# Optimization experiments

Hardware: AMD Instinct MI355X
Metric: run time of the kernel (lower is better)

Reference implementation:

```python
import jax, jax.numpy as jnp
import numpy as np

SIZE = 128
BATCH = 64
STEEPNESS = 10.0


def _odd_even_indices(n):
    """Odd-even transposition sorting network: n layers of disjoint adjacent pairs.
    All layers are padded to k = n//2 pairs with self-pairs (i,i)=(0,0), which are
    exact no-ops under the soft compare-exchange (matches pass-through wires of the
    original network)."""
    k = n // 2
    ia, ib = [], []
    for layer in range(n):
        start = layer % 2
        pa = list(range(start, n - 1, 2))
        pb = [i + 1 for i in pa]
        while len(pa) < k:  # pad with no-op self-pairs
            pa.append(0)
            pb.append(0)
        ia.append(pa)
        ib.append(pb)
    return jnp.asarray(np.array(ia, np.int32)), jnp.asarray(np.array(ib, np.int32))


def setup_inputs() -> dict:
    key = jax.random.key(0)
    return {"vectors": jax.random.normal(key, (BATCH, SIZE), dtype=jnp.float32)}


def _soft_sort(vectors):
    Bsz, n = vectors.shape
    ia, ib = _odd_even_indices(n)  # [n_layers, k] each
    x0 = vectors
    # X[b, i, j] = soft probability mass of input element i at output slot j,
    # i.e. the invariant  x[b] == vectors[b] @ X[b]  holds after every layer.
    X0 = jnp.tile(jnp.eye(n, dtype=vectors.dtype)[None], (Bsz, 1, 1))
    inv_pi = jnp.float32(1.0 / np.pi)

    def step(carry, idx):
        x, X = carry
        a_idx, b_idx = idx
        a = x[:, a_idx]  # [B, k]
        b = x[:, b_idx]  # [B, k]
        # Cauchy CDF relaxation of the comparison (module default distribution)
        alpha = jnp.arctan(STEEPNESS * (b - a)) * inv_pi + 0.5
        x = x.at[:, a_idx].set(alpha * a + (1.0 - alpha) * b)        # soft min
        x = x.at[:, b_idx].set((1.0 - alpha) * a + alpha * b)        # soft max
        A = X[:, :, a_idx]   # [B, n, k] columns feeding the 'a' wires
        Bc = X[:, :, b_idx]  # [B, n, k] columns feeding the 'b' wires
        w = alpha[:, None, :]
        X = X.at[:, :, a_idx].set(w * A + (1.0 - w) * Bc)
        X = X.at[:, :, b_idx].set((1.0 - w) * A + w * Bc)
        return (x, X), None

    (x, X), _ = jax.lax.scan(step, (x0, X0), (ia, ib))
    return x, X


def reference(vectors):
    # Returns (softly sorted values [B, n], relaxed permutation matrix [B, n, n])
    return _soft_sort(vectors)
```

## Files before the change

### kernel.cpp

```cpp
#include <hip/hip_runtime.h>
#include <math.h>

#define SIZE 128
#define BATCH 64
#define STEEP 10.0f
#define INV_PI 0.3183098861837907f

__global__ __launch_bounds__(256) void soft_sort_kernel(
    const float* __restrict__ vec, float* __restrict__ out)
{
    const int tid      = threadIdx.x;
    const int lane     = tid & 63;
    const int wave     = tid >> 6;
    const int batch    = blockIdx.x >> 2;
    const int rowchunk = blockIdx.x & 3;
    const int r_base   = rowchunk * 32 + wave * 8;

    const int c0 = 2 * lane;
    const int c1 = c0 + 1;

    const float2 xv = *reinterpret_cast<const float2*>(vec + batch * SIZE + c0);
    float xa = xv.x, xb = xv.y;

    float XA[8], XB[8];
#pragma unroll
    for (int i = 0; i < 8; ++i) {
        const int row = r_base + i;
        XA[i] = (row == c0) ? 1.0f : 0.0f;
        XB[i] = (row == c1) ? 1.0f : 0.0f;
    }

    const int laneR = (lane < 63) ? lane + 1 : 63;
    const int laneL = (lane > 0)  ? lane - 1 : 0;
    const bool hasR = (lane < 63);
    const bool hasL = (lane > 0);

    for (int layer = 0; layer < SIZE; layer += 2) {
        {
            const float alpha = atanf(STEEP * (xb - xa)) * INV_PI + 0.5f;
            const float t  = alpha * (xa - xb);
            const float na = xb + t;
            xb = xa - t;
            xa = na;
#pragma unroll
            for (int i = 0; i < 8; ++i) {
                const float tr = alpha * (XA[i] - XB[i]);
                const float nA = XB[i] + tr;
                XB[i] = XA[i] - tr;
                XA[i] = nA;
            }
        }
        {
            const float xnext  = __shfl(xa, laneR);
            const float alphaR = atanf(STEEP * (xnext - xb)) * INV_PI + 0.5f;
            const float alphaL = __shfl(alphaR, laneL);
            const float xprev  = __shfl(xb, laneL);

            const float nxb = xnext + alphaR * (xb - xnext);
            const float nxa = xprev + alphaL * (xa - xprev);
            xb = hasR ? nxb : xb;
            xa = hasL ? nxa : xa;
#pragma unroll
            for (int i = 0; i < 8; ++i) {
                const float nA = __shfl(XA[i], laneR);
                const float pB = __shfl(XB[i], laneL);
                const float nXB = nA + alphaR * (XB[i] - nA);
                const float nXA = pB + alphaL * (XA[i] - pB);
                XB[i] = hasR ? nXB : XB[i];
                XA[i] = hasL ? nXA : XA[i];
            }
        }
    }

    float* __restrict__ Xout = out + BATCH * SIZE + batch * SIZE * SIZE;
#pragma unroll
    for (int i = 0; i < 8; ++i) {
        const int row = r_base + i;
        *reinterpret_cast<float2*>(Xout + row * SIZE + c0) = make_float2(XA[i], XB[i]);
    }
    if (rowchunk == 0 && wave == 0) {
        *reinterpret_cast<float2*>(out + batch * SIZE + c0) = make_float2(xa, xb);
    }
}

extern "C" void kernel_launch(void* const* d_in, const int* in_sizes, int n_in,
                              void* d_out, int out_size, void* d_ws, size_t ws_size,
                              hipStream_t stream) {
    const float* vec = (const float*)d_in[0];
    float* out = (float*)d_out;
    (void)in_sizes; (void)n_in; (void)d_ws; (void)ws_size; (void)out_size;

    dim3 grid(BATCH * 4);
    dim3 block(256);
    hipLaunchKernelGGL(soft_sort_kernel, grid, block, 0, stream, vec, out);
}
```

Measured before the change: 79.46 us.

## Split soft sort into alpha precompute and permutation-evolution kernels with polynomial atan

A first kernel runs the value recurrence once per batch and stores all per-layer alphas in workspace, using a minimax polynomial atan approximation instead of atanf. A second kernel evolves the permutation rows with a new layout: each thread holds 8 contiguous columns, so most compare-exchanges happen in registers and only two shuffles are needed per odd layer. This removes the redundant alpha recomputation done by every row-chunk block and most of the cross-lane shuffles. The cost is an extra kernel launch, a global round-trip through the alpha buffer, and approximation error in alpha.

```diff
diff --git a/kernel.cpp b/kernel.cpp
--- a/kernel.cpp
+++ b/kernel.cpp
@@ -4,83 +4,129 @@
 #define SIZE 128
 #define BATCH 64
 #define STEEP 10.0f
-#define INV_PI 0.3183098861837907f
 
-__global__ __launch_bounds__(256) void soft_sort_kernel(
-    const float* __restrict__ vec, float* __restrict__ out)
+__device__ __forceinline__ float alpha_from_delta(float delta) {
+    const float C0 =  0.31830265f;
+    const float C1 = -0.10587730f;
+    const float C2 =  0.06160680f;
+    const float C3 = -0.03706173f;
+    const float C4 =  0.01676007f;
+    const float C5 = -0.00373098f;
+    float t   = STEEP * delta;
+    float at  = fabsf(t);
+    bool  inv = at > 1.0f;
+    float z   = inv ? __builtin_amdgcn_rcpf(at) : at;
+    float z2  = z * z;
+    float q   = C5;
+    q = fmaf(q, z2, C4);
+    q = fmaf(q, z2, C3);
+    q = fmaf(q, z2, C2);
+    q = fmaf(q, z2, C1);
+    q = fmaf(q, z2, C0);
+    q = q * z;
+    float r = inv ? 0.5f - q : q;
+    return (t >= 0.0f) ? (0.5f + r) : (0.5f - r);
+}
+
+__global__ __launch_bounds__(64) void alpha_kernel(
+    const float* __restrict__ vec, float* __restrict__ alpha_buf,
+    float* __restrict__ out)
 {
-    const int tid      = threadIdx.x;
-    const int lane     = tid & 63;
-    const int wave     = tid >> 6;
-    const int batch    = blockIdx.x >> 2;
-    const int rowchunk = blockIdx.x & 3;
-    const int r_base   = rowchunk * 32 + wave * 8;
-
-    const int c0 = 2 * lane;
-    const int c1 = c0 + 1;
+    const int lane  = threadIdx.x;
+    const int batch = blockIdx.x;
+    const int c0    = 2 * lane;
 
     const float2 xv = *reinterpret_cast<const float2*>(vec + batch * SIZE + c0);
     float xa = xv.x, xb = xv.y;
 
-    float XA[8], XB[8];
+    float* __restrict__ ab = alpha_buf + batch * (SIZE * 64);
+    const int  laneR = (lane < 63) ? lane + 1 : 63;
+    const int  laneL = (lane > 0)  ? lane - 1 : 0;
+    const bool hasR  = (lane < 63);
+    const bool hasL  = (lane > 0);
+
+    for (int layer = 0; layer < SIZE; layer += 2) {
+        const float ae = alpha_from_delta(xb - xa);
+        ab[layer * 64 + lane] = ae;
+        const float t  = ae * (xa - xb);
+        const float na = xb + t;
+        xb = xa - t;
+        xa = na;
+        const float xnext = __shfl(xa, laneR);
+        const float ao    = alpha_from_delta(xnext - xb);
+        ab[(layer + 1) * 64 + lane] = ao;
+        const float aoL   = __shfl(ao, laneL);
+        const float xprev = __shfl(xb, laneL);
+        const float nxb = xnext + ao  * (xb - xnext);
+        const float nxa = xprev + aoL * (xa - xprev);
+        xb = hasR ? nxb : xb;
+        xa = hasL ? nxa : xa;
+    }
+    *reinterpret_cast<float2*>(out + batch * SIZE + c0) = make_float2(xa, xb);
+}
+
+__global__ __launch_bounds__(256) void evolve_kernel(
+    const float* __restrict__ alpha_buf, float* __restrict__ out)
+{
+    const int tid     = threadIdx.x;
+    const int lane    = tid & 63;
+    const int wave    = tid >> 6;
+    const int chunk   = lane & 15;
+    const int row_sub = lane >> 4;
+    const int batch   = blockIdx.x >> 3;
+    const int rowgrp  = blockIdx.x & 7;
+    const int row     = rowgrp * 16 + wave * 4 + row_sub;
+    const int c8      = chunk * 8;
+
+    float v[8];
 #pragma unroll
-    for (int i = 0; i < 8; ++i) {
-        const int row = r_base + i;
-        XA[i] = (row == c0) ? 1.0f : 0.0f;
-        XB[i] = (row == c1) ? 1.0f : 0.0f;
+    for (int j = 0; j < 8; ++j) v[j] = (row == c8 + j) ? 1.0f : 0.0f;
+
+    const float* __restrict__ ab = alpha_buf + batch * (SIZE * 64);
+    const int q4 = chunk * 4;
+    const int qm = (q4 > 0) ? q4 - 1 : 0;
+
+    const bool hasR  = (chunk < 15);
+    const bool hasL  = (chunk > 0);
+    const int  laneR = hasR ? lane + 1 : lane;
+    const int  laneL = hasL ? lane - 1 : lane;
+
+    float4 ae = *reinterpret_cast<const float4*>(ab + 0 * 64 + q4);
+    float4 ao = *reinterpret_cast<const float4*>(ab + 1 * 64 + q4);
+    float  aL = ab[1 * 64 + qm];
+
+    for (int L = 0; L < 64; ++L) {
+        const int nxt = (L < 63) ? (2 * L + 2) : (2 * L);
+        const float4 ae_n = *reinterpret_cast<const float4*>(ab + nxt * 64 + q4);
+        const float4 ao_n = *reinterpret_cast<const float4*>(ab + (nxt + 1) * 64 + q4);
+        const float  aL_n = ab[(nxt + 1) * 64 + qm];
+
+        {
+            float A, B, d;
+            A = v[0]; B = v[1]; d = A - B; v[0] = fmaf(ae.x, d, B); v[1] = fmaf(-ae.x, d, A);
+            A = v[2]; B = v[3]; d = A - B; v[2] = fmaf(ae.y, d, B); v[3] = fmaf(-ae.y, d, A);
+            A = v[4]; B = v[5]; d = A - B; v[4] = fmaf(ae.z, d, B); v[5] = fmaf(-ae.z, d, A);
+            A = v[6]; B = v[7]; d = A - B; v[6] = fmaf(ae.w, d, B); v[7] = fmaf(-ae.w, d, A);
+        }
+        const float nb0 = __shfl(v[0], laneR);
+        const float pb7 = __shfl(v[7], laneL);
+        {
+            float A, B, d;
+            A = v[1]; B = v[2]; d = A - B; v[1] = fmaf(ao.x, d, B); v[2] = fmaf(-ao.x, d, A);
+            A = v[3]; B = v[4]; d = A - B; v[3] = fmaf(ao.y, d, B); v[4] = fmaf(-ao.y, d, A);
+            A = v[5]; B = v[6]; d = A - B; v[5] = fmaf(ao.z, d, B); v[6] = fmaf(-ao.z, d, A);
+        }
+        const float r = fmaf(ao.w, v[7] - nb0, nb0);
+        const float l = fmaf(aL, v[0] - pb7, pb7);
+        v[7] = hasR ? r : v[7];
+        v[0] = hasL ? l : v[0];
+
+        ae = ae_n; ao = ao_n; aL = aL_n;
     }
 
-    const int laneR = (lane < 63) ? lane + 1 : 63;
-    const int laneL = (lane > 0)  ? lane - 1 : 0;
-    const bool hasR = (lane < 63);
-    const bool hasL = (lane > 0);
-
-    for (int layer = 0; layer < SIZE; layer += 2) {
-        {
-            const float alpha = atanf(STEEP * (xb - xa)) * INV_PI + 0.5f;
-            const float t  = alpha * (xa - xb);
-            const float na = xb + t;
-            xb = xa - t;
-            xa = na;
-#pragma unroll
-            for (int i = 0; i < 8; ++i) {
-                const float tr = alpha * (XA[i] - XB[i]);
-                const float nA = XB[i] + tr;
-                XB[i] = XA[i] - tr;
-                XA[i] = nA;
-            }
-        }
-        {
-            const float xnext  = __shfl(xa, laneR);
-            const float alphaR = atanf(STEEP * (xnext - xb)) * INV_PI + 0.5f;
-            const float alphaL = __shfl(alphaR, laneL);
-            const float xprev  = __shfl(xb, laneL);
-
-            const float nxb = xnext + alphaR * (xb - xnext);
-            const float nxa = xprev + alphaL * (xa - xprev);
-            xb = hasR ? nxb : xb;
-            xa = hasL ? nxa : xa;
-#pragma unroll
-            for (int i = 0; i < 8; ++i) {
-                const float nA = __shfl(XA[i], laneR);
-                const float pB = __shfl(XB[i], laneL);
-                const float nXB = nA + alphaR * (XB[i] - nA);
-                const float nXA = pB + alphaL * (XA[i] - pB);
-                XB[i] = hasR ? nXB : XB[i];
-                XA[i] = hasL ? nXA : XA[i];
-            }
-        }
-    }
-
-    float* __restrict__ Xout = out + BATCH * SIZE + batch * SIZE * SIZE;
-#pragma unroll
-    for (int i = 0; i < 8; ++i) {
-        const int row = r_base + i;
-        *reinterpret_cast<float2*>(Xout + row * SIZE + c0) = make_float2(XA[i], XB[i]);
-    }
-    if (rowchunk == 0 && wave == 0) {
-        *reinterpret_cast<float2*>(out + batch * SIZE + c0) = make_float2(xa, xb);
-    }
+    float* __restrict__ X = out + BATCH * SIZE + (batch * SIZE + row) * SIZE + c8;
+    *reinterpret_cast<float4*>(X)     = make_float4(v[0], v[1], v[2], v[3]);
+    *reinterpret_cast<float4*>(X + 4) = make_float4(v[4], v[5], v[6], v[7]);
 }
 
 extern "C" void kernel_launch(void* const* d_in, const int* in_sizes, int n_in,
@@ -88,9 +134,11 @@
                               hipStream_t stream) {
     const float* vec = (const float*)d_in[0];
     float* out = (float*)d_out;
-    (void)in_sizes; (void)n_in; (void)d_ws; (void)ws_size; (void)out_size;
+    float* alpha_buf = (float*)d_ws;
+    (void)in_sizes; (void)n_in; (void)ws_size; (void)out_size;
 
-    dim3 grid(BATCH * 4);
-    dim3 block(256);
-    hipLaunchKernelGGL(soft_sort_kernel, grid, block, 0, stream, vec, out);
+    hipLaunchKernelGGL(alpha_kernel, dim3(BATCH), dim3(64), 0, stream,
+                       vec, alpha_buf, out);
+    hipLaunchKernelGGL(evolve_kernel, dim3(BATCH * 8), dim3(256), 0, stream,
+                       alpha_buf, out);
 }
```

Result: slower. 81.93 us (+3.1%).
